# Optimization experiments

Hardware: AMD Instinct MI355X
Metric: run time of the kernel (lower is better)

## Reference

```python
import jax, jax.numpy as jnp
import numpy as np

N_NODES = 50000
N_EDGES = 800000
IN_FEATS, HIDDEN_FEATS, NUM_CLASSES = 64, 64, 32


def setup_inputs() -> dict:
    key = jax.random.key(0)
    ks = jax.random.split(key, 9)
    features = jax.random.normal(ks[0], (N_NODES, IN_FEATS), dtype=jnp.float32)
    src = jax.random.randint(ks[1], (N_EDGES,), 0, N_NODES, dtype=jnp.int32)
    dst = jax.random.randint(ks[2], (N_EDGES,), 0, N_NODES, dtype=jnp.int32)
    def lin(k, fan_in, fan_out):
        bound = 1.0 / np.sqrt(fan_in)
        return jax.random.uniform(k, (fan_in, fan_out), jnp.float32, -bound, bound)
    W_self1 = lin(ks[3], IN_FEATS, HIDDEN_FEATS)
    W_neigh1 = lin(ks[4], IN_FEATS, HIDDEN_FEATS)
    b1 = jnp.zeros((HIDDEN_FEATS,), jnp.float32)
    W_self2 = lin(ks[5], HIDDEN_FEATS, NUM_CLASSES)
    W_neigh2 = lin(ks[6], HIDDEN_FEATS, NUM_CLASSES)
    b2 = jnp.zeros((NUM_CLASSES,), jnp.float32)
    return {"features": features, "W_self1": W_self1, "W_neigh1": W_neigh1, "b1": b1,
            "W_self2": W_self2, "W_neigh2": W_neigh2, "b2": b2, "src": src, "dst": dst}


def _sage_mean(x, W_self, W_neigh, b, src, dst, n_nodes):
    # mean over in-neighbors: edge (u, v) sends x[u] into v
    agg = jax.ops.segment_sum(x[src], dst, num_segments=n_nodes)          # [N, F]
    deg = jax.ops.segment_sum(jnp.ones((src.shape[0],), x.dtype), dst,
                              num_segments=n_nodes)                        # [N]
    h_neigh = agg / jnp.maximum(deg, 1.0)[:, None]                         # zero-in-degree -> 0
    return x @ W_self + h_neigh @ W_neigh + b


def reference(features, W_self1, W_neigh1, b1, W_self2, W_neigh2, b2, src, dst):
    n = features.shape[0]
    h = jax.nn.relu(_sage_mean(features, W_self1, W_neigh1, b1, src, dst, n))
    return _sage_mean(h, W_self2, W_neigh2, b2, src, dst, n)
```

## Files before the change

### kernel.cpp

```cpp
#include <hip/hip_runtime.h>

#define N_NODES 50000
#define N_EDGES 800000
#define NB 196
#define PBLOCKS 256
#define CHUNK 3125
#define GEMM_BLOCKS 782
#define CSR_CAP 4608

typedef unsigned short ushort_t;
typedef __attribute__((ext_vector_type(8))) short bf16x8;
typedef __attribute__((ext_vector_type(4))) float f32x4;


__device__ __forceinline__ float bflo(unsigned int u) {
    return __uint_as_float(u << 16);
}
__device__ __forceinline__ float bfhi(unsigned int u) {
    return __uint_as_float(u & 0xffff0000u);
}
__device__ __forceinline__ ushort_t f2bf(float f) {
    unsigned int x = __float_as_uint(f);
    return (ushort_t)((x + 0x7fffu + ((x >> 16) & 1u)) >> 16);
}
__device__ __forceinline__ unsigned int pack_bf(float lo, float hi) {
    return (unsigned int)f2bf(lo) | ((unsigned int)f2bf(hi) << 16);
}
__device__ __forceinline__ void split_bf(float v, short& hi, short& lo) {
    ushort_t h = f2bf(v);
    float r = v - __uint_as_float((unsigned int)h << 16);
    hi = (short)h;
    lo = (short)f2bf(r);
}

__global__ __launch_bounds__(256)
void gemm128_and_count(const float* __restrict__ A,
                       const float* __restrict__ B1,
                       const float* __restrict__ B2,
                       ushort_t* __restrict__ Cself,
                       ushort_t* __restrict__ Cn,
                       const int* __restrict__ dst,
                       int* __restrict__ blocktot) {
    __shared__ int hist[NB];

    if (blockIdx.x >= GEMM_BLOCKS) {
        const int pb = blockIdx.x - GEMM_BLOCKS;
        for (int i = threadIdx.x; i < NB; i += 256) hist[i] = 0;
        __syncthreads();
        const int e0 = pb * CHUNK;
        const int e1 = e0 + CHUNK;
        for (int e = e0 + (int)threadIdx.x; e < e1; e += 256)
            atomicAdd(&hist[dst[e] >> 8], 1);
        __syncthreads();
        for (int i = threadIdx.x; i < NB; i += 256)
            blocktot[i * PBLOCKS + pb] = hist[i];
        return;
    }

    const int l  = threadIdx.x & 63;
    const int w  = threadIdx.x >> 6;
    const int lr = l & 15;
    const int lk = (l >> 4) << 3;

    bf16x8 bhi[2][2], blo[2][2];
#pragma unroll
    for (int nt = 0; nt < 2; ++nt) {
        const int n = w * 32 + nt * 16 + lr;
        const float* Bp = (n < 64) ? (B1 + n) : (B2 + (n - 64));
#pragma unroll
        for (int ks = 0; ks < 2; ++ks) {
#pragma unroll
            for (int j = 0; j < 8; ++j) {
                float bv = Bp[(size_t)(ks * 32 + lk + j) * 64];
                short h, lo;
                split_bf(bv, h, lo);
                bhi[nt][ks][j] = h;
                blo[nt][ks][j] = lo;
            }
        }
    }

    const int m0 = blockIdx.x * 64;
    f32x4 acc[4][2];
#pragma unroll
    for (int mt = 0; mt < 4; ++mt)
#pragma unroll
        for (int nt = 0; nt < 2; ++nt) {
            f32x4 z = {0.f, 0.f, 0.f, 0.f};
            acc[mt][nt] = z;
        }

#pragma unroll
    for (int mt = 0; mt < 4; ++mt) {
        const int m = m0 + mt * 16 + lr;
        const bool valid = (m < N_NODES);
        const float* Ap = A + (size_t)m * 64 + lk;
#pragma unroll
        for (int ks = 0; ks < 2; ++ks) {
            float4 f0, f1;
            if (valid) {
                f0 = *(const float4*)(Ap + ks * 32);
                f1 = *(const float4*)(Ap + ks * 32 + 4);
            } else {
                f0 = make_float4(0.f, 0.f, 0.f, 0.f);
                f1 = f0;
            }
            const float fv[8] = {f0.x, f0.y, f0.z, f0.w, f1.x, f1.y, f1.z, f1.w};
            bf16x8 ahi, alo;
#pragma unroll
            for (int j = 0; j < 8; ++j) {
                short h, lo;
                split_bf(fv[j], h, lo);
                ahi[j] = h;
                alo[j] = lo;
            }
#pragma unroll
            for (int nt = 0; nt < 2; ++nt) {
                acc[mt][nt] = __builtin_amdgcn_mfma_f32_16x16x32_bf16(
                    ahi, bhi[nt][ks], acc[mt][nt], 0, 0, 0);
                acc[mt][nt] = __builtin_amdgcn_mfma_f32_16x16x32_bf16(
                    alo, bhi[nt][ks], acc[mt][nt], 0, 0, 0);
                acc[mt][nt] = __builtin_amdgcn_mfma_f32_16x16x32_bf16(
                    ahi, blo[nt][ks], acc[mt][nt], 0, 0, 0);
            }
        }
    }

#pragma unroll
    for (int mt = 0; mt < 4; ++mt) {
        const int mbase = m0 + mt * 16 + ((l >> 4) << 2);
#pragma unroll
        for (int nt = 0; nt < 2; ++nt) {
            const int n = w * 32 + nt * 16 + lr;
            ushort_t* T = (n < 64) ? (Cself + n) : (Cn + (n - 64));
#pragma unroll
            for (int r = 0; r < 4; ++r) {
                const int m = mbase + r;
                if (m < N_NODES) T[(size_t)m * 64] = f2bf(acc[mt][nt][r]);
            }
        }
    }
}

__global__ __launch_bounds__(256)
void part_write(const int* __restrict__ src, const int* __restrict__ dst,
                const int* __restrict__ blocktot, unsigned int* __restrict__ brec) {
    __shared__ int ssum[256];
    __shared__ int cur[NB];
    const int pb = blockIdx.x;
    const int t  = threadIdx.x;

    int rsum = 0, mypart = 0;
    if (t < NB) {
        const int* rp = blocktot + t * PBLOCKS;
#pragma unroll 8
        for (int j = 0; j < PBLOCKS; ++j) {
            if (j == pb) mypart = rsum;
            rsum += rp[j];
        }
    }
    ssum[t] = (t < NB) ? rsum : 0;
    __syncthreads();
    for (int off = 1; off < 256; off <<= 1) {
        int add = (t >= off) ? ssum[t - off] : 0;
        __syncthreads();
        ssum[t] += add;
        __syncthreads();
    }
    if (t < NB) cur[t] = (ssum[t] - rsum) + mypart;
    __syncthreads();

    const int e0 = pb * CHUNK;
    const int e1 = e0 + CHUNK;
    for (int e = e0 + t; e < e1; e += 256) {
        int d = dst[e];
        int s = src[e];
        int pos = atomicAdd(&cur[d >> 8], 1);
        brec[pos] = ((unsigned int)(d & 255) << 16) | (unsigned int)s;
    }
}

__global__ __launch_bounds__(1024)
void csr_gather1(const int* __restrict__ blocktot,
                 const unsigned int* __restrict__ brec,
                 int* __restrict__ csr_src, int* __restrict__ row_ptr,
                 const ushort_t* __restrict__ Tself,
                 const ushort_t* __restrict__ Tn,
                 const float* __restrict__ bias,
                 ushort_t* __restrict__ out) {
    __shared__ int ssum[256];
    __shared__ int cnt[256];
    __shared__ int rs[256];
    __shared__ int cur[256];
    __shared__ int csr_lds[CSR_CAP];

    const int b = blockIdx.x;
    const int node0 = b * 256;
    const int t = threadIdx.x;

    if (t < 256) {
        int rsum = 0;
        if (t < NB) {
            const int* rp = blocktot + t * PBLOCKS;
#pragma unroll 8
            for (int j = 0; j < PBLOCKS; ++j) rsum += rp[j];
        }
        ssum[t] = rsum;
        cnt[t] = 0;
    }
    __syncthreads();
    for (int off = 1; off < 256; off <<= 1) {
        int add = (t < 256 && t >= off) ? ssum[t - off] : 0;
        __syncthreads();
        if (t < 256) ssum[t] += add;
        __syncthreads();
    }
    const int w0 = (b == 0) ? 0 : ssum[b - 1];
    const int w1 = ssum[b];
    __syncthreads();

    for (int i = w0 + t; i < w1; i += 1024)
        atomicAdd(&cnt[brec[i] >> 16], 1);
    __syncthreads();

    if (t < 256) cur[t] = cnt[t];
    __syncthreads();
    for (int off = 1; off < 256; off <<= 1) {
        int add = (t < 256 && t >= off) ? cur[t - off] : 0;
        __syncthreads();
        if (t < 256) cur[t] += add;
        __syncthreads();
    }
    if (t < 256) {
        const int excl = cur[t] - cnt[t];
        rs[t] = excl;
        const int node = node0 + t;
        if (node <= N_NODES) row_ptr[node] = w0 + excl;
    }
    __syncthreads();
    if (t < 256) cur[t] = rs[t];
    __syncthreads();

    for (int i = w0 + t; i < w1; i += 1024) {
        const unsigned int r = brec[i];
        const int pos = atomicAdd(&cur[r >> 16], 1);
        const int s = (int)(r & 0xffffu);
        csr_src[w0 + pos] = s;
        if (pos < CSR_CAP) csr_lds[pos] = s;
    }
    __syncthreads();

    const int wv   = t >> 6;
    const int lane = t & 63;
    const int half = lane >> 5;
    const int hl   = lane & 31;
    const int r = hl >> 3;
    const int c = hl & 7;

#define ACC8(u)                                           \
    a[0] += bflo(u.x); a[1] += bfhi(u.x);                 \
    a[2] += bflo(u.y); a[3] += bfhi(u.y);                 \
    a[4] += bflo(u.z); a[5] += bfhi(u.z);                 \
    a[6] += bflo(u.w); a[7] += bfhi(u.w);

    for (int it = 0; it < 8; ++it) {
        const int pair = wv + (it << 4);
        const int dloc = (pair << 1) + half;
        const int v = node0 + dloc;
        if (v >= N_NODES) continue;
        const int sl = rs[dloc];
        const int cn = cnt[dloc];

        float a[8];
#pragma unroll
        for (int i = 0; i < 8; ++i) a[i] = 0.f;

        const int nfast = (cn < 32) ? cn : 32;
        int  sidx[8];
        bool act[8];
#pragma unroll
        for (int j = 0; j < 8; ++j) {
            const int tt = r + (j << 2);
            act[j] = (tt < nfast);
            sidx[j] = 0;
            if (act[j]) {
                const int ad = sl + tt;
                sidx[j] = (ad < CSR_CAP) ? csr_lds[ad] : csr_src[w0 + ad];
            }
        }
        uint4 u[8];
#pragma unroll
        for (int j = 0; j < 8; ++j) {
            u[j] = make_uint4(0u, 0u, 0u, 0u);
            if (act[j]) u[j] = *(const uint4*)&Tn[(size_t)sidx[j] * 64 + c * 8];
        }
#pragma unroll
        for (int j = 0; j < 8; ++j) { ACC8(u[j]) }

        for (int tt = 32 + r; tt < cn; tt += 4) {
            const int ad = sl + tt;
            const int s = (ad < CSR_CAP) ? csr_lds[ad] : csr_src[w0 + ad];
            const uint4 uu = *(const uint4*)&Tn[(size_t)s * 64 + c * 8];
            ACC8(uu)
        }

#pragma unroll
        for (int off = 8; off < 32; off <<= 1) {
#pragma unroll
            for (int i = 0; i < 8; ++i) a[i] += __shfl_xor(a[i], off);
        }

        if (r == 0) {
            const float inv = 1.0f / (float)max(cn, 1);
            uint4 su = *(const uint4*)&Tself[(size_t)v * 64 + c * 8];
            float4 bA = *(const float4*)&bias[c * 8];
            float4 bB = *(const float4*)&bias[c * 8 + 4];
            float o[8];
            o[0] = bflo(su.x) + a[0] * inv + bA.x;
            o[1] = bfhi(su.x) + a[1] * inv + bA.y;
            o[2] = bflo(su.y) + a[2] * inv + bA.z;
            o[3] = bfhi(su.y) + a[3] * inv + bA.w;
            o[4] = bflo(su.z) + a[4] * inv + bB.x;
            o[5] = bfhi(su.z) + a[5] * inv + bB.y;
            o[6] = bflo(su.w) + a[6] * inv + bB.z;
            o[7] = bfhi(su.w) + a[7] * inv + bB.w;
#pragma unroll
            for (int i = 0; i < 8; ++i) o[i] = fmaxf(o[i], 0.f);
            uint4 p;
            p.x = pack_bf(o[0], o[1]); p.y = pack_bf(o[2], o[3]);
            p.z = pack_bf(o[4], o[5]); p.w = pack_bf(o[6], o[7]);
            *(uint4*)&out[(size_t)v * 64 + c * 8] = p;
        }
    }
#undef ACC8
}

__global__ __launch_bounds__(256)
void gemm_cat64_bf16(const ushort_t* __restrict__ A,
                     const float* __restrict__ B1,
                     const float* __restrict__ B2,
                     ushort_t* __restrict__ Cself,
                     ushort_t* __restrict__ Cn) {
    const int l  = threadIdx.x & 63;
    const int w  = threadIdx.x >> 6;
    const int lr = l & 15;
    const int lk = (l >> 4) << 3;

    const int n = w * 16 + lr;
    const float* Bp = (n < 32) ? (B1 + n) : (B2 + (n - 32));
    bf16x8 bhi[2], blo[2];
#pragma unroll
    for (int ks = 0; ks < 2; ++ks) {
#pragma unroll
        for (int j = 0; j < 8; ++j) {
            float bv = Bp[(size_t)(ks * 32 + lk + j) * 32];
            short h, lo;
            split_bf(bv, h, lo);
            bhi[ks][j] = h;
            blo[ks][j] = lo;
        }
    }

    const int m0 = blockIdx.x * 64;
    f32x4 acc[4];
#pragma unroll
    for (int mt = 0; mt < 4; ++mt) {
        f32x4 z = {0.f, 0.f, 0.f, 0.f};
        acc[mt] = z;
    }

#pragma unroll
    for (int mt = 0; mt < 4; ++mt) {
        const int m = m0 + mt * 16 + lr;
        const bool valid = (m < N_NODES);
#pragma unroll
        for (int ks = 0; ks < 2; ++ks) {
            bf16x8 a;
            if (valid) {
                a = *(const bf16x8*)&A[(size_t)m * 64 + ks * 32 + lk];
            } else {
                bf16x8 z = {0, 0, 0, 0, 0, 0, 0, 0};
                a = z;
            }
            acc[mt] = __builtin_amdgcn_mfma_f32_16x16x32_bf16(a, bhi[ks], acc[mt], 0, 0, 0);
            acc[mt] = __builtin_amdgcn_mfma_f32_16x16x32_bf16(a, blo[ks], acc[mt], 0, 0, 0);
        }
    }

    ushort_t* T = (n < 32) ? (Cself + n) : (Cn + (n - 32));
#pragma unroll
    for (int mt = 0; mt < 4; ++mt) {
        const int mbase = m0 + mt * 16 + ((l >> 4) << 2);
#pragma unroll
        for (int r = 0; r < 4; ++r) {
            const int m = mbase + r;
            if (m < N_NODES) T[(size_t)m * 32] = f2bf(acc[mt][r]);
        }
    }
}

__global__ __launch_bounds__(256)
void gather2(const ushort_t* __restrict__ Tself,
             const ushort_t* __restrict__ Tn,
             const int* __restrict__ row_ptr,
             const int* __restrict__ csr_src, const float* __restrict__ bias,
             float* __restrict__ out) {
    constexpr int F = 32;
    constexpr int LPR = 4;
    constexpr int G = 4;
    constexpr int MAXJ = 8;
    const int lane = threadIdx.x & 63;
    const int q  = lane >> 4;
    const int hl = lane & 15;
    const int r = hl >> 2;
    const int c = hl & 3;
    const int v = (((int)blockIdx.x * (int)blockDim.x + (int)threadIdx.x) >> 6) * 4 + q;
    if (v >= N_NODES) return;
    const int start = row_ptr[v];
    const int cnt   = row_ptr[v + 1] - start;

    float a[8];
#pragma unroll
    for (int i = 0; i < 8; ++i) a[i] = 0.f;

#define ACC8(u)                                           \
    a[0] += bflo(u.x); a[1] += bfhi(u.x);                 \
    a[2] += bflo(u.y); a[3] += bfhi(u.y);                 \
    a[4] += bflo(u.z); a[5] += bfhi(u.z);                 \
    a[6] += bflo(u.w); a[7] += bfhi(u.w);

    int idx0 = 0, idx1 = 0;
    if (hl < cnt)      idx0 = csr_src[start + hl];
    if (16 + hl < cnt) idx1 = csr_src[start + 16 + hl];

    const int nfast = (cnt < 32) ? cnt : 32;
    int  sidx[MAXJ];
    bool act[MAXJ];
#pragma unroll
    for (int j = 0; j < MAXJ; ++j) {
        const int t = r + j * G;
        act[j] = (t < nfast);
        sidx[j] = (j < 4) ? __shfl(idx0, q * 16 + t)
                          : __shfl(idx1, q * 16 + (t - 16));
    }
    uint4 u[MAXJ];
#pragma unroll
    for (int j = 0; j < MAXJ; ++j) {
        u[j] = make_uint4(0u, 0u, 0u, 0u);
        if (act[j]) u[j] = *(const uint4*)&Tn[(size_t)sidx[j] * F + c * 8];
    }
#pragma unroll
    for (int j = 0; j < MAXJ; ++j) { ACC8(u[j]) }

    for (int t = 32 + r; t < cnt; t += G) {
        const int s = csr_src[start + t];
        uint4 uu = *(const uint4*)&Tn[(size_t)s * F + c * 8];
        ACC8(uu)
    }
#undef ACC8

#pragma unroll
    for (int off = LPR; off < 16; off <<= 1) {
#pragma unroll
        for (int i = 0; i < 8; ++i) a[i] += __shfl_xor(a[i], off);
    }

    if (r == 0) {
        const float inv = 1.0f / (float)max(cnt, 1);
        uint4 su = *(const uint4*)&Tself[(size_t)v * F + c * 8];
        float4 bA = *(const float4*)&bias[c * 8];
        float4 bB = *(const float4*)&bias[c * 8 + 4];
        float o[8];
        o[0] = bflo(su.x) + a[0] * inv + bA.x;
        o[1] = bfhi(su.x) + a[1] * inv + bA.y;
        o[2] = bflo(su.y) + a[2] * inv + bA.z;
        o[3] = bfhi(su.y) + a[3] * inv + bA.w;
        o[4] = bflo(su.z) + a[4] * inv + bB.x;
        o[5] = bfhi(su.z) + a[5] * inv + bB.y;
        o[6] = bflo(su.w) + a[6] * inv + bB.z;
        o[7] = bfhi(su.w) + a[7] * inv + bB.w;
        *(float4*)&out[(size_t)v * F + c * 8]     = make_float4(o[0], o[1], o[2], o[3]);
        *(float4*)&out[(size_t)v * F + c * 8 + 4] = make_float4(o[4], o[5], o[6], o[7]);
    }
}

extern "C" void kernel_launch(void* const* d_in, const int* in_sizes, int n_in,
                              void* d_out, int out_size, void* d_ws, size_t ws_size,
                              hipStream_t stream) {
    const float* features = (const float*)d_in[0];
    const float* W_self1  = (const float*)d_in[1];
    const float* W_neigh1 = (const float*)d_in[2];
    const float* b1       = (const float*)d_in[3];
    const float* W_self2  = (const float*)d_in[4];
    const float* W_neigh2 = (const float*)d_in[5];
    const float* b2       = (const float*)d_in[6];
    const int*   src      = (const int*)d_in[7];
    const int*   dst      = (const int*)d_in[8];

    ushort_t* Tself1 = (ushort_t*)d_ws;
    ushort_t* Tn1    = Tself1 + (size_t)N_NODES * 64;
    ushort_t* h      = Tn1 + (size_t)N_NODES * 64;
    int* row_ptr     = (int*)(h + (size_t)N_NODES * 64);
    int* csr_src     = row_ptr + (N_NODES + 1);
    unsigned int* brec = (unsigned int*)(csr_src + N_EDGES);
    int* blocktot    = (int*)(brec + N_EDGES);

    ushort_t* Tself2 = Tself1;
    ushort_t* Tn2    = Tself1 + (size_t)N_NODES * 32;

    gemm128_and_count<<<GEMM_BLOCKS + PBLOCKS, 256, 0, stream>>>(
        features, W_self1, W_neigh1, Tself1, Tn1, dst, blocktot);
    part_write<<<PBLOCKS, 256, 0, stream>>>(src, dst, blocktot, brec);
    csr_gather1<<<NB, 1024, 0, stream>>>(
        blocktot, brec, csr_src, row_ptr, Tself1, Tn1, b1, h);
    gemm_cat64_bf16<<<GEMM_BLOCKS, 256, 0, stream>>>(h, W_self2, W_neigh2, Tself2, Tn2);
    gather2<<<(N_NODES + 15) / 16, 256, 0, stream>>>(
        Tself2, Tn2, row_ptr, csr_src, b2, (float*)d_out);
}
```

Measured before the change: 161.3 us.

## Fuse layer-2 GEMM into CSR gather kernel via LDS-resident hidden tile

Each CSR/gather block now writes its 256 ReLU hidden rows into an LDS tile instead of global memory. After a barrier, its 16 waves multiply that tile by W_self2/W_neigh2 with split-bf16 MFMA and write the layer-2 projections directly. This removes a kernel launch and the global write and read of the hidden matrix. The cost is about 40KB of extra LDS per 1024-thread block, which may reduce occupancy, plus each block re-splitting the weights. Tself2/Tn2 move to their own workspace region so they no longer alias Tself1.

Measured after the change: 158.4 us. No clear change (-1.8%).

```diff
diff --git a/kernel.cpp b/kernel.cpp
--- a/kernel.cpp
+++ b/kernel.cpp
@@ -7,6 +7,7 @@
 #define CHUNK 3125
 #define GEMM_BLOCKS 782
 #define CSR_CAP 4608
+#define HST 80
 
 typedef unsigned short ushort_t;
 typedef __attribute__((ext_vector_type(8))) short bf16x8;
@@ -181,22 +182,31 @@
 }
 
 __global__ __launch_bounds__(1024)
-void csr_gather1(const int* __restrict__ blocktot,
-                 const unsigned int* __restrict__ brec,
-                 int* __restrict__ csr_src, int* __restrict__ row_ptr,
-                 const ushort_t* __restrict__ Tself,
-                 const ushort_t* __restrict__ Tn,
-                 const float* __restrict__ bias,
-                 ushort_t* __restrict__ out) {
+void csr_gather1_g2(const int* __restrict__ blocktot,
+                    const unsigned int* __restrict__ brec,
+                    int* __restrict__ csr_src, int* __restrict__ row_ptr,
+                    const ushort_t* __restrict__ Tself,
+                    const ushort_t* __restrict__ Tn,
+                    const float* __restrict__ bias,
+                    const float* __restrict__ Ws2,
+                    const float* __restrict__ Wn2,
+                    ushort_t* __restrict__ Tself2,
+                    ushort_t* __restrict__ Tn2) {
     __shared__ int ssum[256];
     __shared__ int cnt[256];
     __shared__ int rs[256];
     __shared__ int cur[256];
     __shared__ int csr_lds[CSR_CAP];
+    __shared__ ushort_t h_lds[256 * HST];
 
     const int b = blockIdx.x;
     const int node0 = b * 256;
     const int t = threadIdx.x;
+
+    {
+        unsigned int* hz = (unsigned int*)h_lds;
+        for (int i = t; i < 256 * HST / 2; i += 1024) hz[i] = 0u;
+    }
 
     if (t < 256) {
         int rsum = 0;
@@ -329,72 +339,58 @@
             uint4 p;
             p.x = pack_bf(o[0], o[1]); p.y = pack_bf(o[2], o[3]);
             p.z = pack_bf(o[4], o[5]); p.w = pack_bf(o[6], o[7]);
-            *(uint4*)&out[(size_t)v * 64 + c * 8] = p;
+            *(uint4*)&h_lds[dloc * HST + c * 8] = p;
         }
     }
 #undef ACC8
-}
-
-__global__ __launch_bounds__(256)
-void gemm_cat64_bf16(const ushort_t* __restrict__ A,
-                     const float* __restrict__ B1,
-                     const float* __restrict__ B2,
-                     ushort_t* __restrict__ Cself,
-                     ushort_t* __restrict__ Cn) {
-    const int l  = threadIdx.x & 63;
-    const int w  = threadIdx.x >> 6;
-    const int lr = l & 15;
-    const int lk = (l >> 4) << 3;
-
-    const int n = w * 16 + lr;
-    const float* Bp = (n < 32) ? (B1 + n) : (B2 + (n - 32));
-    bf16x8 bhi[2], blo[2];
+    __syncthreads();
+
+    const int lr  = lane & 15;
+    const int lk2 = (lane >> 4) << 3;
+
+    bf16x8 bhi[4][2], blo[4][2];
+#pragma unroll
+    for (int nt = 0; nt < 4; ++nt) {
+        const int n = nt * 16 + lr;
+        const float* Bp = (n < 32) ? (Ws2 + n) : (Wn2 + (n - 32));
+#pragma unroll
+        for (int ks = 0; ks < 2; ++ks) {
+#pragma unroll
+            for (int j = 0; j < 8; ++j) {
+                float bv = Bp[(size_t)(ks * 32 + lk2 + j) * 32];
+                short h, lo;
+                split_bf(bv, h, lo);
+                bhi[nt][ks][j] = h;
+                blo[nt][ks][j] = lo;
+            }
+        }
+    }
+
+    f32x4 acc2[4];
+#pragma unroll
+    for (int nt = 0; nt < 4; ++nt) {
+        f32x4 z = {0.f, 0.f, 0.f, 0.f};
+        acc2[nt] = z;
+    }
 #pragma unroll
     for (int ks = 0; ks < 2; ++ks) {
-#pragma unroll
-        for (int j = 0; j < 8; ++j) {
-            float bv = Bp[(size_t)(ks * 32 + lk + j) * 32];
-            short h, lo;
-            split_bf(bv, h, lo);
-            bhi[ks][j] = h;
-            blo[ks][j] = lo;
-        }
-    }
-
-    const int m0 = blockIdx.x * 64;
-    f32x4 acc[4];
-#pragma unroll
-    for (int mt = 0; mt < 4; ++mt) {
-        f32x4 z = {0.f, 0.f, 0.f, 0.f};
-        acc[mt] = z;
-    }
-
-#pragma unroll
-    for (int mt = 0; mt < 4; ++mt) {
-        const int m = m0 + mt * 16 + lr;
-        const bool valid = (m < N_NODES);
-#pragma unroll
-        for (int ks = 0; ks < 2; ++ks) {
-            bf16x8 a;
-            if (valid) {
-                a = *(const bf16x8*)&A[(size_t)m * 64 + ks * 32 + lk];
-            } else {
-                bf16x8 z = {0, 0, 0, 0, 0, 0, 0, 0};
-                a = z;
-            }
-            acc[mt] = __builtin_amdgcn_mfma_f32_16x16x32_bf16(a, bhi[ks], acc[mt], 0, 0, 0);
-            acc[mt] = __builtin_amdgcn_mfma_f32_16x16x32_bf16(a, blo[ks], acc[mt], 0, 0, 0);
-        }
-    }
-
-    ushort_t* T = (n < 32) ? (Cself + n) : (Cn + (n - 32));
-#pragma unroll
-    for (int mt = 0; mt < 4; ++mt) {
-        const int mbase = m0 + mt * 16 + ((l >> 4) << 2);
-#pragma unroll
-        for (int r = 0; r < 4; ++r) {
-            const int m = mbase + r;
-            if (m < N_NODES) T[(size_t)m * 32] = f2bf(acc[mt][r]);
+        const bf16x8 a = *(const bf16x8*)&h_lds[(wv * 16 + lr) * HST + ks * 32 + lk2];
+#pragma unroll
+        for (int nt = 0; nt < 4; ++nt) {
+            acc2[nt] = __builtin_amdgcn_mfma_f32_16x16x32_bf16(a, bhi[nt][ks], acc2[nt], 0, 0, 0);
+            acc2[nt] = __builtin_amdgcn_mfma_f32_16x16x32_bf16(a, blo[nt][ks], acc2[nt], 0, 0, 0);
+        }
+    }
+
+    const int mbase = node0 + wv * 16 + ((lane >> 4) << 2);
+#pragma unroll
+    for (int nt = 0; nt < 4; ++nt) {
+        const int n = nt * 16 + lr;
+        ushort_t* T = (n < 32) ? (Tself2 + n) : (Tn2 + (n - 32));
+#pragma unroll
+        for (int rr = 0; rr < 4; ++rr) {
+            const int m = mbase + rr;
+            if (m < N_NODES) T[(size_t)m * 32] = f2bf(acc2[nt][rr]);
         }
     }
 }
@@ -499,21 +495,21 @@
 
     ushort_t* Tself1 = (ushort_t*)d_ws;
     ushort_t* Tn1    = Tself1 + (size_t)N_NODES * 64;
-    ushort_t* h      = Tn1 + (size_t)N_NODES * 64;
-    int* row_ptr     = (int*)(h + (size_t)N_NODES * 64);
+    ushort_t* T2     = Tn1 + (size_t)N_NODES * 64;
+    int* row_ptr     = (int*)(T2 + (size_t)N_NODES * 64);
     int* csr_src     = row_ptr + (N_NODES + 1);
     unsigned int* brec = (unsigned int*)(csr_src + N_EDGES);
     int* blocktot    = (int*)(brec + N_EDGES);
 
-    ushort_t* Tself2 = Tself1;
-    ushort_t* Tn2    = Tself1 + (size_t)N_NODES * 32;
+    ushort_t* Tself2 = T2;
+    ushort_t* Tn2    = T2 + (size_t)N_NODES * 32;
 
     gemm128_and_count<<<GEMM_BLOCKS + PBLOCKS, 256, 0, stream>>>(
         features, W_self1, W_neigh1, Tself1, Tn1, dst, blocktot);
     part_write<<<PBLOCKS, 256, 0, stream>>>(src, dst, blocktot, brec);
-    csr_gather1<<<NB, 1024, 0, stream>>>(
-        blocktot, brec, csr_src, row_ptr, Tself1, Tn1, b1, h);
-    gemm_cat64_bf16<<<GEMM_BLOCKS, 256, 0, stream>>>(h, W_self2, W_neigh2, Tself2, Tn2);
+    csr_gather1_g2<<<NB, 1024, 0, stream>>>(
+        blocktot, brec, csr_src, row_ptr, Tself1, Tn1, b1,
+        W_self2, W_neigh2, Tself2, Tn2);
     gather2<<<(N_NODES + 15) / 16, 256, 0, stream>>>(
         Tself2, Tn2, row_ptr, csr_src, b2, (float*)d_out);
 }
```
